# Kernel optimization log

Measured on AMD Instinct MI355X. Metric: run time of the kernel, lower is better.

## Reference

```python
import jax, jax.numpy as jnp
import numpy as np

B, K, D, H = 16384, 3, 1024, 16
DH = D // H  # head_dim = 64


def setup_inputs() -> dict:
    key = jax.random.key(0)
    ks = jax.random.split(key, 12)
    s = 1.0 / np.sqrt(D)
    inp = {
        "tokens": jax.random.normal(ks[0], (B, K, D), dtype=jnp.float32),
        "ctx": jax.random.normal(ks[1], (B, 1, D), dtype=jnp.float32),
        "Wq": jax.random.uniform(ks[2], (D, D), jnp.float32, -s, s),
        "bq": jnp.zeros((D,), jnp.float32),
        "Wk": jax.random.uniform(ks[3], (D, D), jnp.float32, -s, s),
        "bk": jnp.zeros((D,), jnp.float32),
        "Wv": jax.random.uniform(ks[4], (D, D), jnp.float32, -s, s),
        "bv": jnp.zeros((D,), jnp.float32),
        "Wc": jax.random.uniform(ks[5], (D, D), jnp.float32, -s, s),
        "bc": jnp.zeros((D,), jnp.float32),
        "Wo": jax.random.uniform(ks[6], (D, D), jnp.float32, -s, s),
        "bo": jnp.zeros((D,), jnp.float32),
    }
    return inp


def _split_heads(x):
    # (B, L, D) -> (B, H, L, DH)
    Bq, L, _ = x.shape
    return x.reshape(Bq, L, H, DH).transpose(0, 2, 1, 3)


def reference(tokens, ctx, Wq, bq, Wk, bk, Wv, bv, Wc, bc, Wo, bo):
    q = _split_heads(tokens @ Wq.T + bq)          # (B,H,K,DH)
    k = _split_heads(tokens @ Wk.T + bk)          # (B,H,K,DH)
    v = _split_heads(tokens @ Wv.T + bv)          # (B,H,K,DH)
    c = _split_heads(ctx @ Wc.T + bc)             # (B,H,1,DH)
    k_ctx = k * c                                  # context-modulated keys
    v_ctx = v * c                                  # context-modulated values
    scores = jnp.einsum("bhqd,bhkd->bhqk", q, k_ctx) / jnp.sqrt(jnp.float32(DH))
    probs = jax.nn.softmax(scores, axis=-1)       # dropout p=0.0 -> identity
    out = jnp.einsum("bhqk,bhkd->bhqd", probs, v_ctx)
    out = out.transpose(0, 2, 1, 3).reshape(tokens.shape[0], K, D)  # merge heads
    return out @ Wo.T + bo
```

## Files before the change

### kernel.cpp

```cpp
#include <hip/hip_runtime.h>
#include <hip/hip_bf16.h>

#define BB 16384
#define KK 3
#define DD 1024
#define HH 16

typedef __attribute__((ext_vector_type(8))) short bf16x8;
typedef __attribute__((ext_vector_type(4))) float f32x4;
typedef unsigned int u32;

__device__ __forceinline__ void load_lds16(const void* g, void* l) {
  __builtin_amdgcn_global_load_lds(
      (const __attribute__((address_space(1))) u32*)g,
      (__attribute__((address_space(3))) u32*)l,
      16, 0, 0);
}

__device__ __forceinline__ unsigned short f2bf(float f) {
  __hip_bfloat16 h = __float2bfloat16(f);
  unsigned short u;
  __builtin_memcpy(&u, &h, 2);
  return u;
}

__device__ __forceinline__ float bf2f(unsigned short u) {
  union { float f; u32 i; } cv;
  cv.i = ((u32)u) << 16;
  return cv.f;
}

__global__ __launch_bounds__(256)
void cast_inputs(const float* __restrict__ tokens, const float* __restrict__ ctx,
                 unsigned short* __restrict__ Xb, unsigned short* __restrict__ Cin) {
  const int nTok4 = BB * KK * DD / 4;
  const int nTot4 = nTok4 + BB * DD / 4;
  const int stride = gridDim.x * blockDim.x;
  for (int i = blockIdx.x * blockDim.x + threadIdx.x; i < nTot4; i += stride) {
    float4 v;
    if (i < nTok4) v = ((const float4*)tokens)[i];
    else           v = ((const float4*)ctx)[i - nTok4];
    ushort4 o;
    o.x = f2bf(v.x); o.y = f2bf(v.y); o.z = f2bf(v.z); o.w = f2bf(v.w);
    if (i < nTok4) ((ushort4*)Xb)[i] = o;
    else           ((ushort4*)Cin)[i - nTok4] = o;
  }
}

__global__ __launch_bounds__(256)
void cast_weights5(const float* __restrict__ Wq, const float* __restrict__ Wk,
                   const float* __restrict__ Wv, const float* __restrict__ Wc,
                   const float* __restrict__ Wo,
                   unsigned short* __restrict__ Wqkv,
                   unsigned short* __restrict__ Wcb,
                   unsigned short* __restrict__ Wob) {
  const int mat = blockIdx.x >> 8;
  const int inner = blockIdx.x & 255;
  const float* src = mat == 0 ? Wq : mat == 1 ? Wk : mat == 2 ? Wv
                   : mat == 3 ? Wc : Wo;
  unsigned short* dst = mat <= 2 ? Wqkv + (size_t)mat * DD * DD
                      : mat == 3 ? Wcb : Wob;
  const int base = inner * 1024 + threadIdx.x;
#pragma unroll
  for (int k = 0; k < 4; ++k) {
    const int i = base + k * 256;
    float4 v = ((const float4*)src)[i];
    ushort4 o;
    o.x = f2bf(v.x); o.y = f2bf(v.y); o.z = f2bf(v.z); o.w = f2bf(v.w);
    ((ushort4*)dst)[i] = o;
  }
}

template <bool OUT_F32>
__device__ __forceinline__ void gemm_body(char* lds,
    const __hip_bfloat16* __restrict__ A, const __hip_bfloat16* __restrict__ Bt,
    const float* __restrict__ bias, int biasOff, void* __restrict__ Cout,
    int tm, int tn, int N, int K) {
  const int tid = threadIdx.x;
  const int l = tid & 63;
  const int w = tid >> 6;
  const int wm = w >> 2;
  const int wn = w & 3;
  const int l15 = l & 15;
  const int g = l >> 4;
  const int l7 = l15 & 7;

  const int aBase = (l15 << 7) + (((wm << 2) + g) ^ l7) * 16;
  const int bBase = 16384 + ((((wn & 1) << 6) + l15) << 7) +
                    ((((wn >> 1) << 2) + g) ^ l7) * 16;

  const size_t strideK = (size_t)K * 2;
  const char* Ab = (const char*)A + (size_t)tm * 256 * strideK;
  const char* Bb = (const char*)Bt + (size_t)tn * 256 * strideK;
  const int q = (tid & 7) ^ ((tid >> 3) & 7);
  const size_t g0 = (size_t)((q >> 2) * 128 + (tid >> 3)) * strideK + (q & 3) * 16;
  const size_t g1 = g0 + (size_t)64 * strideK;
  const int sld = tid << 4;

  f32x4 acc[8][4] = {};
  const int nkt = K >> 5;

#define STAGE_AB(T)                                                       \
  {                                                                       \
    char* sb = lds + (((T) & 3) << 15);                                   \
    const char* ga = Ab + ((size_t)(T) << 6);                             \
    const char* gb = Bb + ((size_t)(T) << 6);                             \
    load_lds16(ga + g0, sb + sld);                                        \
    load_lds16(ga + g1, sb + 8192 + sld);                                 \
    load_lds16(gb + g0, sb + 16384 + sld);                                \
    load_lds16(gb + g1, sb + 24576 + sld);                                \
  }

  STAGE_AB(0);
  STAGE_AB(1);
  STAGE_AB(2);

  for (int kt = 0; kt < nkt; ++kt) {
    if (kt <= nkt - 3)
      asm volatile("s_waitcnt vmcnt(8)" ::: "memory");
    else if (kt == nkt - 2)
      asm volatile("s_waitcnt vmcnt(4)" ::: "memory");
    else
      asm volatile("s_waitcnt vmcnt(0)" ::: "memory");
    __builtin_amdgcn_s_barrier();
    asm volatile("" ::: "memory");

    const char* slot = lds + ((kt & 3) << 15);
    bf16x8 bfr[4], af[8];
#pragma unroll
    for (int n = 0; n < 4; ++n)
      bfr[n] = *(const bf16x8*)(slot + bBase + (n << 11));
#pragma unroll
    for (int m = 0; m < 8; ++m)
      af[m] = *(const bf16x8*)(slot + aBase + (m << 11));

    if (kt + 3 < nkt) STAGE_AB(kt + 3);

    __builtin_amdgcn_s_setprio(1);
#pragma unroll
    for (int m = 0; m < 8; ++m)
#pragma unroll
      for (int n = 0; n < 4; ++n)
        acc[m][n] = __builtin_amdgcn_mfma_f32_16x16x32_bf16(af[m], bfr[n],
                                                            acc[m][n], 0, 0, 0);
    __builtin_amdgcn_s_setprio(0);
  }
#undef STAGE_AB

  const int cbase = tn * 256 + (wn << 6) + l15;
  float b4[4];
#pragma unroll
  for (int n = 0; n < 4; ++n) b4[n] = bias[cbase + (n << 4) - biasOff];
  const size_t rbase = (size_t)tm * 256 + (wm << 7) + ((l >> 4) << 2);
#pragma unroll
  for (int m = 0; m < 8; ++m) {
#pragma unroll
    for (int j = 0; j < 4; ++j) {
      const size_t row = rbase + (m << 4) + j;
#pragma unroll
      for (int n = 0; n < 4; ++n) {
        const int col = cbase + (n << 4);
        float v = acc[m][n][j] + b4[n];
        if (OUT_F32)
          ((float*)Cout)[row * N + col] = v;
        else
          ((unsigned short*)Cout)[row * N + col] = f2bf(v);
      }
    }
  }
}

__global__ __launch_bounds__(512, 2)
void gemm_all(const __hip_bfloat16* __restrict__ Xq,
              const __hip_bfloat16* __restrict__ Wqkv,
              const float* __restrict__ bq, const float* __restrict__ bk,
              const float* __restrict__ bv,
              unsigned short* __restrict__ QKV,
              const __hip_bfloat16* __restrict__ Cin,
              const __hip_bfloat16* __restrict__ Wcb,
              const float* __restrict__ bc,
              unsigned short* __restrict__ Cpr) {
  __shared__ __align__(128) char lds[131072];
  const int nwgQ = (BB * KK / 256) * (3 * DD / 256);
  const int nwg = nwgQ + (BB / 256) * (DD / 256);
  int bid = blockIdx.x;
  bid = (bid & 7) * (nwg >> 3) + (bid >> 3);
  if (bid < nwgQ) {
    const int tm = bid / 12, tn = bid % 12;
    const int which = tn >> 2;
    const float* bp = which == 0 ? bq : which == 1 ? bk : bv;
    gemm_body<false>(lds, Xq, Wqkv, bp, which << 10, QKV, tm, tn, 3 * DD, DD);
  } else {
    const int b2 = bid - nwgQ;
    gemm_body<false>(lds, Cin, Wcb, bc, 0, Cpr, b2 / 4, b2 % 4, DD, DD);
  }
}

__global__ __launch_bounds__(512, 2)
void gemm_out(const __hip_bfloat16* __restrict__ A,
              const __hip_bfloat16* __restrict__ Wob,
              const float* __restrict__ bo, float* __restrict__ C) {
  __shared__ __align__(128) char lds[131072];
  const int nwg = (BB * KK / 256) * (DD / 256);
  int bid = blockIdx.x;
  bid = (bid & 7) * (nwg >> 3) + (bid >> 3);
  gemm_body<true>(lds, A, Wob, bo, 0, C, bid / 4, bid % 4, DD, DD);
}

__global__ __launch_bounds__(256)
void attn_kernel(const unsigned short* __restrict__ QKV,
                 const unsigned short* __restrict__ Cp,
                 unsigned short* __restrict__ Out) {
  const int t = threadIdx.x;
  const int grp = (blockIdx.x << 4) + (t >> 4);
  const int x = t & 15;
  const int b = grp >> 4;
  const int h = grp & 15;

  const size_t col = (size_t)h * 64 + (x << 2);
  const size_t qbase = (size_t)b * 3 * 3072 + col;

  ushort4 cu = *(const ushort4*)&Cp[(size_t)b * 1024 + col];
  float c[4] = {bf2f(cu.x), bf2f(cu.y), bf2f(cu.z), bf2f(cu.w)};

  float q[3][4], kc[3][4], vc[3][4];
#pragma unroll
  for (int i = 0; i < 3; ++i) {
    ushort4 qu = *(const ushort4*)&QKV[qbase + (size_t)i * 3072];
    ushort4 ku = *(const ushort4*)&QKV[qbase + (size_t)i * 3072 + 1024];
    ushort4 vu = *(const ushort4*)&QKV[qbase + (size_t)i * 3072 + 2048];
    q[i][0] = bf2f(qu.x); q[i][1] = bf2f(qu.y); q[i][2] = bf2f(qu.z); q[i][3] = bf2f(qu.w);
    kc[i][0] = bf2f(ku.x) * c[0]; kc[i][1] = bf2f(ku.y) * c[1];
    kc[i][2] = bf2f(ku.z) * c[2]; kc[i][3] = bf2f(ku.w) * c[3];
    vc[i][0] = bf2f(vu.x) * c[0]; vc[i][1] = bf2f(vu.y) * c[1];
    vc[i][2] = bf2f(vu.z) * c[2]; vc[i][3] = bf2f(vu.w) * c[3];
  }

  float s[9];
#pragma unroll
  for (int i = 0; i < 3; ++i)
#pragma unroll
    for (int j = 0; j < 3; ++j)
      s[i * 3 + j] = q[i][0] * kc[j][0] + q[i][1] * kc[j][1] +
                     q[i][2] * kc[j][2] + q[i][3] * kc[j][3];

#pragma unroll
  for (int off = 8; off > 0; off >>= 1)
#pragma unroll
    for (int e = 0; e < 9; ++e)
      s[e] += __shfl_xor(s[e], off, 64);

  const float scale = 0.125f;
#pragma unroll
  for (int i = 0; i < 3; ++i) {
    float s0 = s[i * 3 + 0] * scale;
    float s1 = s[i * 3 + 1] * scale;
    float s2 = s[i * 3 + 2] * scale;
    float m = fmaxf(fmaxf(s0, s1), s2);
    float p0 = expf(s0 - m), p1 = expf(s1 - m), p2 = expf(s2 - m);
    float inv = 1.0f / (p0 + p1 + p2);
    ushort4 o;
    o.x = f2bf((p0 * vc[0][0] + p1 * vc[1][0] + p2 * vc[2][0]) * inv);
    o.y = f2bf((p0 * vc[0][1] + p1 * vc[1][1] + p2 * vc[2][1]) * inv);
    o.z = f2bf((p0 * vc[0][2] + p1 * vc[1][2] + p2 * vc[2][2]) * inv);
    o.w = f2bf((p0 * vc[0][3] + p1 * vc[1][3] + p2 * vc[2][3]) * inv);
    *(ushort4*)&Out[(size_t)(b * 3 + i) * 1024 + col] = o;
  }
}

extern "C" void kernel_launch(void* const* d_in, const int* in_sizes, int n_in,
                              void* d_out, int out_size, void* d_ws, size_t ws_size,
                              hipStream_t stream) {
  const float* tokens = (const float*)d_in[0];
  const float* ctx    = (const float*)d_in[1];
  const float* Wq     = (const float*)d_in[2];
  const float* bq     = (const float*)d_in[3];
  const float* Wk     = (const float*)d_in[4];
  const float* bk     = (const float*)d_in[5];
  const float* Wv     = (const float*)d_in[6];
  const float* bv     = (const float*)d_in[7];
  const float* Wc     = (const float*)d_in[8];
  const float* bc     = (const float*)d_in[9];
  const float* Wo     = (const float*)d_in[10];
  const float* bo     = (const float*)d_in[11];

  const int M  = BB * KK;
  const int Mc = BB;
  const int D  = DD;

  char* p = (char*)d_ws;
  auto carve = [&](size_t bytes) {
    char* r = p;
    p += (bytes + 255) & ~(size_t)255;
    return r;
  };
  unsigned short* Xb   = (unsigned short*)carve((size_t)M * D * 2);
  unsigned short* Cin  = (unsigned short*)carve((size_t)Mc * D * 2);
  unsigned short* Wqkv = (unsigned short*)carve((size_t)3 * D * D * 2);
  unsigned short* Wcb  = (unsigned short*)carve((size_t)D * D * 2);
  unsigned short* Wob  = (unsigned short*)carve((size_t)D * D * 2);
  unsigned short* QKV  = (unsigned short*)carve((size_t)M * 3 * D * 2);
  unsigned short* Cpr  = (unsigned short*)carve((size_t)Mc * D * 2);

  hipLaunchKernelGGL(cast_inputs, dim3(4096), dim3(256), 0, stream,
                     tokens, ctx, Xb, Cin);
  hipLaunchKernelGGL(cast_weights5, dim3(1280), dim3(256), 0, stream,
                     Wq, Wk, Wv, Wc, Wo, Wqkv, Wcb, Wob);
  hipLaunchKernelGGL(gemm_all, dim3(2560), dim3(512), 0, stream,
                     (const __hip_bfloat16*)Xb, (const __hip_bfloat16*)Wqkv,
                     bq, bk, bv, QKV,
                     (const __hip_bfloat16*)Cin, (const __hip_bfloat16*)Wcb,
                     bc, Cpr);
  hipLaunchKernelGGL(attn_kernel, dim3(BB * HH / 16), dim3(256), 0, stream,
                     QKV, Cpr, Xb);
  hipLaunchKernelGGL(gemm_out, dim3(768), dim3(512), 0, stream,
                     (const __hip_bfloat16*)Xb, (const __hip_bfloat16*)Wob,
                     bo, (float*)d_out);
}
```

Measured before the change: 642.4 us.

## Switch GEMMs to 32x32x16 MFMA, split ctx GEMM, widen attention and cast vectors

Replaces the 16x16x32 bf16 MFMA tiling in the shared GEMM body with 32x32x16 MFMA, which needs fewer LDS fragment reads per FLOP, and remaps the output epilogue to the 32x32 accumulator layout. Splits the fused QKV+context GEMM launch into two separate kernels. Widens the attention kernel to 8 elements per thread with 128-bit loads and fewer shuffle steps. Rewrites the input cast as a fixed-grid, unrolled, branch-free loop. The new LDS swizzle indexing risks bank conflicts or layout mistakes, and the extra launch adds a small serial gap.

```diff
diff --git a/kernel.cpp b/kernel.cpp
--- a/kernel.cpp
+++ b/kernel.cpp
@@ -8,6 +8,7 @@
 
 typedef __attribute__((ext_vector_type(8))) short bf16x8;
 typedef __attribute__((ext_vector_type(4))) float f32x4;
+typedef __attribute__((ext_vector_type(16))) float f32x16;
 typedef unsigned int u32;
 
 __device__ __forceinline__ void load_lds16(const void* g, void* l) {
@@ -33,17 +34,18 @@
 __global__ __launch_bounds__(256)
 void cast_inputs(const float* __restrict__ tokens, const float* __restrict__ ctx,
                  unsigned short* __restrict__ Xb, unsigned short* __restrict__ Cin) {
-  const int nTok4 = BB * KK * DD / 4;
-  const int nTot4 = nTok4 + BB * DD / 4;
-  const int stride = gridDim.x * blockDim.x;
-  for (int i = blockIdx.x * blockDim.x + threadIdx.x; i < nTot4; i += stride) {
-    float4 v;
-    if (i < nTok4) v = ((const float4*)tokens)[i];
-    else           v = ((const float4*)ctx)[i - nTok4];
+  const bool isCtx = blockIdx.x >= 3072;
+  const float* src = isCtx ? ctx : tokens;
+  unsigned short* dst = isCtx ? Cin : Xb;
+  const int inner = isCtx ? (blockIdx.x - 3072) : blockIdx.x;
+  const int base = inner * 4096 + threadIdx.x;
+#pragma unroll
+  for (int k = 0; k < 16; ++k) {
+    const int i = base + k * 256;
+    float4 v = ((const float4*)src)[i];
     ushort4 o;
     o.x = f2bf(v.x); o.y = f2bf(v.y); o.z = f2bf(v.z); o.w = f2bf(v.w);
-    if (i < nTok4) ((ushort4*)Xb)[i] = o;
-    else           ((ushort4*)Cin)[i - nTok4] = o;
+    ((ushort4*)dst)[i] = o;
   }
 }
 
@@ -72,7 +74,7 @@
 }
 
 template <bool OUT_F32>
-__device__ __forceinline__ void gemm_body(char* lds,
+__device__ __forceinline__ void gemm_body32(char* lds,
     const __hip_bfloat16* __restrict__ A, const __hip_bfloat16* __restrict__ Bt,
     const float* __restrict__ bias, int biasOff, void* __restrict__ Cout,
     int tm, int tn, int N, int K) {
@@ -81,13 +83,11 @@
   const int w = tid >> 6;
   const int wm = w >> 2;
   const int wn = w & 3;
-  const int l15 = l & 15;
-  const int g = l >> 4;
-  const int l7 = l15 & 7;
-
-  const int aBase = (l15 << 7) + (((wm << 2) + g) ^ l7) * 16;
-  const int bBase = 16384 + ((((wn & 1) << 6) + l15) << 7) +
-                    ((((wn >> 1) << 2) + g) ^ l7) * 16;
+  const int l31 = l & 31;
+  const int hk = l >> 5;
+  const int l7 = l31 & 7;
+
+  const int aLine = l31 << 7;
 
   const size_t strideK = (size_t)K * 2;
   const char* Ab = (const char*)A + (size_t)tm * 256 * strideK;
@@ -97,7 +97,7 @@
   const size_t g1 = g0 + (size_t)64 * strideK;
   const int sld = tid << 4;
 
-  f32x4 acc[8][4] = {};
+  f32x16 acc[4][2] = {};
   const int nkt = K >> 5;
 
 #define STAGE_AB(T)                                                       \
@@ -126,41 +126,54 @@
     asm volatile("" ::: "memory");
 
     const char* slot = lds + ((kt & 3) << 15);
-    bf16x8 bfr[4], af[8];
-#pragma unroll
-    for (int n = 0; n < 4; ++n)
-      bfr[n] = *(const bf16x8*)(slot + bBase + (n << 11));
-#pragma unroll
-    for (int m = 0; m < 8; ++m)
-      af[m] = *(const bf16x8*)(slot + aBase + (m << 11));
+    bf16x8 af[4][2], bfr[2][2];
+#pragma unroll
+    for (int n = 0; n < 2; ++n) {
+      const int cIdx = (wn << 1) + n;
+      const char* bp = slot + 16384 + (((cIdx & 3) << 5) << 7) + aLine;
+#pragma unroll
+      for (int s = 0; s < 2; ++s)
+        bfr[n][s] = *(const bf16x8*)(bp +
+            (((((cIdx >> 2) << 2) + (s << 1) + hk) ^ l7) << 4));
+    }
+#pragma unroll
+    for (int m = 0; m < 4; ++m) {
+      const char* ap = slot + ((m << 5) << 7) + aLine;
+#pragma unroll
+      for (int s = 0; s < 2; ++s)
+        af[m][s] = *(const bf16x8*)(ap +
+            ((((wm << 2) + (s << 1) + hk) ^ l7) << 4));
+    }
 
     if (kt + 3 < nkt) STAGE_AB(kt + 3);
 
     __builtin_amdgcn_s_setprio(1);
 #pragma unroll
-    for (int m = 0; m < 8; ++m)
-#pragma unroll
-      for (int n = 0; n < 4; ++n)
-        acc[m][n] = __builtin_amdgcn_mfma_f32_16x16x32_bf16(af[m], bfr[n],
-                                                            acc[m][n], 0, 0, 0);
+    for (int s = 0; s < 2; ++s)
+#pragma unroll
+      for (int m = 0; m < 4; ++m)
+#pragma unroll
+        for (int n = 0; n < 2; ++n)
+          acc[m][n] = __builtin_amdgcn_mfma_f32_32x32x16_bf16(
+              af[m][s], bfr[n][s], acc[m][n], 0, 0, 0);
     __builtin_amdgcn_s_setprio(0);
   }
 #undef STAGE_AB
 
-  const int cbase = tn * 256 + (wn << 6) + l15;
-  float b4[4];
-#pragma unroll
-  for (int n = 0; n < 4; ++n) b4[n] = bias[cbase + (n << 4) - biasOff];
-  const size_t rbase = (size_t)tm * 256 + (wm << 7) + ((l >> 4) << 2);
-#pragma unroll
-  for (int m = 0; m < 8; ++m) {
-#pragma unroll
-    for (int j = 0; j < 4; ++j) {
-      const size_t row = rbase + (m << 4) + j;
-#pragma unroll
-      for (int n = 0; n < 4; ++n) {
-        const int col = cbase + (n << 4);
-        float v = acc[m][n][j] + b4[n];
+  const int cb0 = tn * 256 + (wn << 6) + l31;
+  float b2[2];
+#pragma unroll
+  for (int n = 0; n < 2; ++n) b2[n] = bias[cb0 + (n << 5) - biasOff];
+  const size_t rbase = (size_t)tm * 256 + (wm << 7) + (hk << 2);
+#pragma unroll
+  for (int m = 0; m < 4; ++m) {
+#pragma unroll
+    for (int j = 0; j < 16; ++j) {
+      const size_t row = rbase + (m << 5) + (j & 3) + ((j >> 2) << 3);
+#pragma unroll
+      for (int n = 0; n < 2; ++n) {
+        const int col = cb0 + (n << 5);
+        float v = acc[m][n][j] + b2[n];
         if (OUT_F32)
           ((float*)Cout)[row * N + col] = v;
         else
@@ -171,40 +184,42 @@
 }
 
 __global__ __launch_bounds__(512, 2)
-void gemm_all(const __hip_bfloat16* __restrict__ Xq,
+void gemm_qkv(const __hip_bfloat16* __restrict__ Xb,
               const __hip_bfloat16* __restrict__ Wqkv,
               const float* __restrict__ bq, const float* __restrict__ bk,
               const float* __restrict__ bv,
-              unsigned short* __restrict__ QKV,
-              const __hip_bfloat16* __restrict__ Cin,
+              unsigned short* __restrict__ QKV) {
+  __shared__ __align__(128) char lds[131072];
+  const int nwg = (BB * KK / 256) * (3 * DD / 256);
+  int bid = blockIdx.x;
+  bid = (bid & 7) * (nwg >> 3) + (bid >> 3);
+  const int tm = bid / 12, tn = bid % 12;
+  const int which = tn >> 2;
+  const float* bp = which == 0 ? bq : which == 1 ? bk : bv;
+  gemm_body32<false>(lds, Xb, Wqkv, bp, which << 10, QKV, tm, tn, 3 * DD, DD);
+}
+
+__global__ __launch_bounds__(512, 2)
+void gemm_ctx(const __hip_bfloat16* __restrict__ Cin,
               const __hip_bfloat16* __restrict__ Wcb,
               const float* __restrict__ bc,
               unsigned short* __restrict__ Cpr) {
   __shared__ __align__(128) char lds[131072];
-  const int nwgQ = (BB * KK / 256) * (3 * DD / 256);
-  const int nwg = nwgQ + (BB / 256) * (DD / 256);
+  const int nwg = (BB / 256) * (DD / 256);
   int bid = blockIdx.x;
   bid = (bid & 7) * (nwg >> 3) + (bid >> 3);
-  if (bid < nwgQ) {
-    const int tm = bid / 12, tn = bid % 12;
-    const int which = tn >> 2;
-    const float* bp = which == 0 ? bq : which == 1 ? bk : bv;
-    gemm_body<false>(lds, Xq, Wqkv, bp, which << 10, QKV, tm, tn, 3 * DD, DD);
-  } else {
-    const int b2 = bid - nwgQ;
-    gemm_body<false>(lds, Cin, Wcb, bc, 0, Cpr, b2 / 4, b2 % 4, DD, DD);
-  }
+  gemm_body32<false>(lds, Cin, Wcb, bc, 0, Cpr, bid / 4, bid % 4, DD, DD);
 }
 
 __global__ __launch_bounds__(512, 2)
-void gemm_out(const __hip_bfloat16* __restrict__ A,
-              const __hip_bfloat16* __restrict__ Wob,
-              const float* __restrict__ bo, float* __restrict__ C) {
+void gemm_outp(const __hip_bfloat16* __restrict__ A,
+               const __hip_bfloat16* __restrict__ Wob,
+               const float* __restrict__ bo, float* __restrict__ C) {
   __shared__ __align__(128) char lds[131072];
   const int nwg = (BB * KK / 256) * (DD / 256);
   int bid = blockIdx.x;
   bid = (bid & 7) * (nwg >> 3) + (bid >> 3);
-  gemm_body<true>(lds, A, Wob, bo, 0, C, bid / 4, bid % 4, DD, DD);
+  gemm_body32<true>(lds, A, Wob, bo, 0, C, bid / 4, bid % 4, DD, DD);
 }
 
 __global__ __launch_bounds__(256)
@@ -212,40 +227,46 @@
                  const unsigned short* __restrict__ Cp,
                  unsigned short* __restrict__ Out) {
   const int t = threadIdx.x;
-  const int grp = (blockIdx.x << 4) + (t >> 4);
-  const int x = t & 15;
+  const int grp = (blockIdx.x << 5) + (t >> 3);
+  const int x = t & 7;
   const int b = grp >> 4;
   const int h = grp & 15;
 
-  const size_t col = (size_t)h * 64 + (x << 2);
+  const size_t col = (size_t)h * 64 + (x << 3);
   const size_t qbase = (size_t)b * 3 * 3072 + col;
 
-  ushort4 cu = *(const ushort4*)&Cp[(size_t)b * 1024 + col];
-  float c[4] = {bf2f(cu.x), bf2f(cu.y), bf2f(cu.z), bf2f(cu.w)};
-
-  float q[3][4], kc[3][4], vc[3][4];
+  bf16x8 cu = *(const bf16x8*)&Cp[(size_t)b * 1024 + col];
+  float c[8];
+#pragma unroll
+  for (int d = 0; d < 8; ++d) c[d] = bf2f((unsigned short)cu[d]);
+
+  float q[3][8], kc[3][8], vc[3][8];
 #pragma unroll
   for (int i = 0; i < 3; ++i) {
-    ushort4 qu = *(const ushort4*)&QKV[qbase + (size_t)i * 3072];
-    ushort4 ku = *(const ushort4*)&QKV[qbase + (size_t)i * 3072 + 1024];
-    ushort4 vu = *(const ushort4*)&QKV[qbase + (size_t)i * 3072 + 2048];
-    q[i][0] = bf2f(qu.x); q[i][1] = bf2f(qu.y); q[i][2] = bf2f(qu.z); q[i][3] = bf2f(qu.w);
-    kc[i][0] = bf2f(ku.x) * c[0]; kc[i][1] = bf2f(ku.y) * c[1];
-    kc[i][2] = bf2f(ku.z) * c[2]; kc[i][3] = bf2f(ku.w) * c[3];
-    vc[i][0] = bf2f(vu.x) * c[0]; vc[i][1] = bf2f(vu.y) * c[1];
-    vc[i][2] = bf2f(vu.z) * c[2]; vc[i][3] = bf2f(vu.w) * c[3];
+    bf16x8 qu = *(const bf16x8*)&QKV[qbase + (size_t)i * 3072];
+    bf16x8 ku = *(const bf16x8*)&QKV[qbase + (size_t)i * 3072 + 1024];
+    bf16x8 vu = *(const bf16x8*)&QKV[qbase + (size_t)i * 3072 + 2048];
+#pragma unroll
+    for (int d = 0; d < 8; ++d) {
+      q[i][d] = bf2f((unsigned short)qu[d]);
+      kc[i][d] = bf2f((unsigned short)ku[d]) * c[d];
+      vc[i][d] = bf2f((unsigned short)vu[d]) * c[d];
+    }
   }
 
   float s[9];
 #pragma unroll
   for (int i = 0; i < 3; ++i)
 #pragma unroll
-    for (int j = 0; j < 3; ++j)
-      s[i * 3 + j] = q[i][0] * kc[j][0] + q[i][1] * kc[j][1] +
-                     q[i][2] * kc[j][2] + q[i][3] * kc[j][3];
-
-#pragma unroll
-  for (int off = 8; off > 0; off >>= 1)
+    for (int j = 0; j < 3; ++j) {
+      float acc = 0.f;
+#pragma unroll
+      for (int d = 0; d < 8; ++d) acc += q[i][d] * kc[j][d];
+      s[i * 3 + j] = acc;
+    }
+
+#pragma unroll
+  for (int off = 4; off > 0; off >>= 1)
 #pragma unroll
     for (int e = 0; e < 9; ++e)
       s[e] += __shfl_xor(s[e], off, 64);
@@ -259,12 +280,11 @@
     float m = fmaxf(fmaxf(s0, s1), s2);
     float p0 = expf(s0 - m), p1 = expf(s1 - m), p2 = expf(s2 - m);
     float inv = 1.0f / (p0 + p1 + p2);
-    ushort4 o;
-    o.x = f2bf((p0 * vc[0][0] + p1 * vc[1][0] + p2 * vc[2][0]) * inv);
-    o.y = f2bf((p0 * vc[0][1] + p1 * vc[1][1] + p2 * vc[2][1]) * inv);
-    o.z = f2bf((p0 * vc[0][2] + p1 * vc[1][2] + p2 * vc[2][2]) * inv);
-    o.w = f2bf((p0 * vc[0][3] + p1 * vc[1][3] + p2 * vc[2][3]) * inv);
-    *(ushort4*)&Out[(size_t)(b * 3 + i) * 1024 + col] = o;
+    bf16x8 o;
+#pragma unroll
+    for (int d = 0; d < 8; ++d)
+      o[d] = (short)f2bf((p0 * vc[0][d] + p1 * vc[1][d] + p2 * vc[2][d]) * inv);
+    *(bf16x8*)&Out[(size_t)(b * 3 + i) * 1024 + col] = o;
   }
 }
 
@@ -306,14 +326,15 @@
                      tokens, ctx, Xb, Cin);
   hipLaunchKernelGGL(cast_weights5, dim3(1280), dim3(256), 0, stream,
                      Wq, Wk, Wv, Wc, Wo, Wqkv, Wcb, Wob);
-  hipLaunchKernelGGL(gemm_all, dim3(2560), dim3(512), 0, stream,
+  hipLaunchKernelGGL(gemm_qkv, dim3(2304), dim3(512), 0, stream,
                      (const __hip_bfloat16*)Xb, (const __hip_bfloat16*)Wqkv,
-                     bq, bk, bv, QKV,
+                     bq, bk, bv, QKV);
+  hipLaunchKernelGGL(gemm_ctx, dim3(256), dim3(512), 0, stream,
                      (const __hip_bfloat16*)Cin, (const __hip_bfloat16*)Wcb,
                      bc, Cpr);
-  hipLaunchKernelGGL(attn_kernel, dim3(BB * HH / 16), dim3(256), 0, stream,
+  hipLaunchKernelGGL(attn_kernel, dim3(BB * HH / 32), dim3(256), 0, stream,
                      QKV, Cpr, Xb);
-  hipLaunchKernelGGL(gemm_out, dim3(768), dim3(512), 0, stream,
+  hipLaunchKernelGGL(gemm_outp, dim3(768), dim3(512), 0, stream,
                      (const __hip_bfloat16*)Xb, (const __hip_bfloat16*)Wob,
                      bo, (float*)d_out);
 }
```

After: 662.6 us. 3.1% more time.
